# Kernel optimization log

Hardware: AMD Instinct MI355X
Metric: run time of the kernel (lower is better)

The kernel has to match this reference:

```python
import jax, jax.numpy as jnp
import numpy as np

NC = 80
REG = 16          # DFL bins per coordinate
CONF_THRES = 0.25
IOU_THRES = 0.45
MAX_DET = 300
TOPK = 1000       # fixed-size pre-NMS candidate pool (stand-in for max_nms=30000 with A=8400)
MAX_WH = 7680.0   # class offset for class-aware NMS
LEVELS = [(80, 80, 8.0), (40, 40, 16.0), (20, 20, 32.0)]  # (h, w, stride) for imgsz=640


def _make_anchors():
    """make_anchors: grid-cell centers (+0.5 offset) and per-anchor strides."""
    pts, strs = [], []
    for h, w, s in LEVELS:
        sx = jnp.arange(w, dtype=jnp.float32) + 0.5
        sy = jnp.arange(h, dtype=jnp.float32) + 0.5
        gy, gx = jnp.meshgrid(sy, sx, indexing='ij')
        pts.append(jnp.stack([gx, gy], -1).reshape(-1, 2))
        strs.append(jnp.full((h * w,), s, dtype=jnp.float32))
    return jnp.concatenate(pts).T, jnp.concatenate(strs)  # [2, A], [A]


def _box_iou(b):  # b: [K, 4] xyxy -> [K, K] pairwise IoU
    area = (b[:, 2] - b[:, 0]) * (b[:, 3] - b[:, 1])
    lt = jnp.maximum(b[:, None, :2], b[None, :, :2])
    rb = jnp.minimum(b[:, None, 2:], b[None, :, 2:])
    wh = jnp.clip(rb - lt, 0.0)
    inter = wh[..., 0] * wh[..., 1]
    return inter / (area[:, None] + area[None, :] - inter + 1e-7)


def _nms_keep(iou, valid):
    """Greedy NMS over score-sorted candidates: keep[i] iff valid and no earlier kept box overlaps > thr."""
    K = iou.shape[0]
    idx = jnp.arange(K)
    def body(keep, i):
        sup = jnp.any((iou[i] > IOU_THRES) & keep & (idx < i))
        return keep.at[i].set(valid[i] & jnp.logical_not(sup)), None
    keep, _ = jax.lax.scan(body, jnp.zeros(K, dtype=bool), idx)
    return keep


def _forward(preds, dfl_w):
    B, C, A = preds.shape
    # DFL decode: softmax over 16 bins, expectation with arange(16) weights (the 1x1 conv)
    box_logits = preds[:, :4 * REG].reshape(B, 4, REG, A)
    dist = jnp.einsum('bqra,r->bqa', jax.nn.softmax(box_logits, axis=2), dfl_w)  # [B,4,A] ltrb
    anc, strd = _make_anchors()
    lt, rb = dist[:, :2], dist[:, 2:]
    x1y1 = anc[None] - lt
    x2y2 = anc[None] + rb
    c_xy = (x1y1 + x2y2) / 2
    wh = x2y2 - x1y1
    dbox = jnp.concatenate([c_xy, wh], axis=1) * strd  # dist2bbox(xywh) * stride, [B,4,A]
    cls = jax.nn.sigmoid(preds[:, 4 * REG:])           # [B,NC,A]
    # xywh2xyxy
    cx, cy, w, h = dbox[:, 0], dbox[:, 1], dbox[:, 2], dbox[:, 3]
    boxes = jnp.stack([cx - w / 2, cy - h / 2, cx + w / 2, cy + h / 2], axis=-1)  # [B,A,4]
    conf = jnp.max(cls, axis=1)      # [B,A]
    j = jnp.argmax(cls, axis=1)      # [B,A]
    score = jnp.where(conf > CONF_THRES, conf, -1.0)
    top_s, top_i = jax.lax.top_k(score, TOPK)                               # [B,K]
    tb = jnp.take_along_axis(boxes, top_i[..., None], axis=1)               # [B,K,4]
    tj = jnp.take_along_axis(j, top_i, axis=1)                              # [B,K]
    valid = top_s > CONF_THRES
    ob = tb + (tj.astype(preds.dtype) * MAX_WH)[..., None]                  # class-offset boxes
    iou = jax.vmap(_box_iou)(ob)                                            # [B,K,K]
    keep = jax.vmap(_nms_keep)(iou, valid)                                  # [B,K]
    sel = jnp.where(keep, top_s, -1e9)
    order = jnp.argsort(-sel, axis=1)[:, :MAX_DET]                          # kept, score-sorted
    fb = jnp.take_along_axis(tb, order[..., None], axis=1)
    fs = jnp.take_along_axis(top_s, order, axis=1)
    fj = jnp.take_along_axis(tj, order, axis=1).astype(preds.dtype)
    fv = jnp.take_along_axis(keep, order, axis=1)
    out = jnp.concatenate([fb, fs[..., None], fj[..., None]], axis=-1)
    return out * fv[..., None].astype(preds.dtype)                          # [B,300,6]


def setup_inputs() -> dict:
    key = jax.random.key(0)
    k1, _ = jax.random.split(key)
    preds = jax.random.normal(k1, (32, 4 * REG + NC, 8400), dtype=jnp.float32)
    dfl_w = jnp.arange(REG, dtype=jnp.float32)
    return {"preds": preds, "dfl_w": dfl_w}


def reference(preds, dfl_w):
    return _forward(preds, dfl_w)
```

## Files before the change

### kernel.cpp

```cpp
#include <hip/hip_runtime.h>
#include <cstdint>
#include <cstddef>

typedef unsigned long long u64;
typedef unsigned int u32;

#define A_TOT   8400
#define NCLS    80
#define KSLOT   1024
#define NCHUNK  9
#define TOPK_N  1000
#define MAXDET  300
#define OUT_STRIDE (MAXDET * 6)

#define GLOBAL_AS const __attribute__((address_space(1))) void*
#define LDS_AS __attribute__((address_space(3))) void*


__device__ __forceinline__ float sig32(float x) {
#pragma clang fp contract(off)
    float e = (float)exp(-(double)x);
    float t = 1.0f + e;
    return 1.0f / t;
}

__device__ __forceinline__ u32 key_hi_from_score(float s) {
    u32 u = __float_as_uint(s);
    return (u & 0x80000000u) ? ~u : (u | 0x80000000u);
}
__device__ __forceinline__ float score_from_key_hi(u32 t) {
    u32 u = (t & 0x80000000u) ? (t ^ 0x80000000u) : ~t;
    return __uint_as_float(u);
}

__device__ __forceinline__ u64 mp_rank(const u64* A, const u64* B, int t) {
    int lo = 0, hi = t;
    while (lo < hi) {
        int mid = (lo + hi + 1) >> 1;
        if (A[mid - 1] > B[t - mid]) lo = mid; else hi = mid - 1;
    }
    int i = lo, j = t - lo;
    u64 av = A[i], bv = B[j];
    return av > bv ? av : bv;
}

__global__ __launch_bounds__(256) void k_decode(const float* __restrict__ preds,
                                                u64* __restrict__ key_raw,
                                                float4* __restrict__ dbox) {
#pragma clang fp contract(off)
    __shared__ float tile[2][16][256];
    int b = blockIdx.y;
    int a0 = blockIdx.x * 256;
    int t = threadIdx.x;
    int a = a0 + t;
    int nA = A_TOT - a0; if (nA > 256) nA = 256;
    int p4max = nA >> 2;
    const float* pb = preds + (size_t)b * 144 * A_TOT;

    int l  = t & 63;
    int wv = t >> 6;
    int lc = (l < p4max) ? l : (p4max - 1);

    auto stage = [&](int ch0, int buf) {
#pragma unroll
        for (int k = 0; k < 4; ++k) {
            int r = 4 * k + wv;
            const float* gsrc = pb + (size_t)(ch0 + r) * A_TOT + a0 + 4 * lc;
            __builtin_amdgcn_global_load_lds((GLOBAL_AS)gsrc,
                                             (LDS_AS)&tile[buf][r][0],
                                             16, 0, 0);
        }
    };

    float d[4] = {0.f, 0.f, 0.f, 0.f};
    float m = -3.0e38f, m2 = -3.0e38f;
    int jm = 0;

    stage(0, 0);
    __syncthreads();

    for (int cb = 0; cb < 9; ++cb) {
        int buf = cb & 1;
        if (cb + 1 < 9) stage((cb + 1) * 16, (cb + 1) & 1);
        if (t < nA) {
            float x[16];
#pragma unroll
            for (int r = 0; r < 16; ++r) x[r] = tile[buf][r][t];
            if (cb < 4) {
                float mx = x[0];
#pragma unroll
                for (int r = 1; r < 16; ++r) mx = fmaxf(mx, x[r]);
                float e[16], s = 0.f;
#pragma unroll
                for (int r = 0; r < 16; ++r) { e[r] = expf(x[r] - mx); s = s + e[r]; }
                float dd = 0.f;
#pragma unroll
                for (int r = 0; r < 16; ++r) { float pr = e[r] / s; dd = dd + pr * (float)r; }
                d[cb] = dd;
            } else {
                int cbase = (cb - 4) * 16;
#pragma unroll
                for (int r = 0; r < 16; ++r) {
                    int c = cbase + r;
                    float v = x[r];
                    if (v > m) { m2 = m; m = v; jm = c; }
                    else if (v > m2) { m2 = v; }
                }
            }
        }
        if (cb < 8) __syncthreads();
    }

    if (t >= nA) return;

    const float* pc = pb + (size_t)64 * A_TOT + a;
    float conf; int cls = jm;
    if ((m - m2) < 1e-4f || m > 7.0f) {
        float sb = -1.0f; int jb = 0;
        for (int c = 0; c < NCLS; ++c) {
            float s = sig32(pc[(size_t)c * A_TOT]);
            if (s > sb) { sb = s; jb = c; }
        }
        conf = sb; cls = jb;
    } else {
        conf = sig32(m);
    }
    float score = (conf > 0.25f) ? conf : -1.0f;
    u32 hi = key_hi_from_score(score);
    u32 lo = ((0x3FFFu - (u32)a) << 7) | (u32)cls;
    key_raw[(size_t)b * A_TOT + a] = ((u64)hi << 32) | lo;

    int row, col; float stride;
    if (a < 6400)      { row = a / 80;          col = a % 80;          stride = 8.0f; }
    else if (a < 8000) { int aa = a - 6400; row = aa / 40; col = aa % 40; stride = 16.0f; }
    else               { int aa = a - 8000; row = aa / 20; col = aa % 20; stride = 32.0f; }
    float ax = (float)col + 0.5f;
    float ay = (float)row + 0.5f;
    float x1 = ax - d[0], y1 = ay - d[1];
    float x2 = ax + d[2], y2 = ay + d[3];
    float cx = (x1 + x2) / 2.0f, cy = (y1 + y2) / 2.0f;
    float w  = x2 - x1,          h  = y2 - y1;
    float4 db;
    db.x = cx * stride; db.y = cy * stride; db.z = w * stride; db.w = h * stride;
    dbox[(size_t)b * A_TOT + a] = db;
}

__global__ __launch_bounds__(1024) void k_chunksort(const u64* __restrict__ key_raw,
                                                    u64* __restrict__ key_sorted) {
    __shared__ u64 s[KSLOT];
    int b = blockIdx.y, ch = blockIdx.x, t = threadIdx.x;
    int a = ch * KSLOT + t;
    s[t] = (a < A_TOT) ? key_raw[(size_t)b * A_TOT + a] : 0ull;
    __syncthreads();
    for (int k = 2; k <= KSLOT; k <<= 1) {
        for (int j = k >> 1; j > 0; j >>= 1) {
            int ixj = t ^ j;
            if (ixj > t) {
                u64 x = s[t], y = s[ixj];
                bool descBlock = ((t & k) == 0);
                bool sw = descBlock ? (x < y) : (x > y);
                if (sw) { s[t] = y; s[ixj] = x; }
            }
            __syncthreads();
        }
    }
    key_sorted[((size_t)b * NCHUNK + ch) * KSLOT + t] = s[t];
}

__global__ __launch_bounds__(1024) void k_select(const u64* __restrict__ key_sorted,
                                                 u64* __restrict__ topk,
                                                 const float4* __restrict__ dbox,
                                                 float* __restrict__ tb,
                                                 float* __restrict__ ob,
                                                 float* __restrict__ area,
                                                 u32* __restrict__ validf) {
#pragma clang fp contract(off)
    __shared__ u64 L[5 * KSLOT];
    int b = blockIdx.x, t = threadIdx.x;
    const u64* KS = key_sorted + (size_t)b * NCHUNK * KSLOT;

    u64 r0 = mp_rank(KS + 0 * KSLOT, KS + 1 * KSLOT, t);
    u64 r1 = mp_rank(KS + 2 * KSLOT, KS + 3 * KSLOT, t);
    u64 r2 = mp_rank(KS + 4 * KSLOT, KS + 5 * KSLOT, t);
    u64 r3 = mp_rank(KS + 6 * KSLOT, KS + 7 * KSLOT, t);
    u64 r4 = KS[8 * KSLOT + t];
    L[0 * KSLOT + t] = r0; L[1 * KSLOT + t] = r1;
    L[2 * KSLOT + t] = r2; L[3 * KSLOT + t] = r3;
    L[4 * KSLOT + t] = r4;
    __syncthreads();

    u64 m0 = mp_rank(L + 0 * KSLOT, L + 1 * KSLOT, t);
    u64 m1 = mp_rank(L + 2 * KSLOT, L + 3 * KSLOT, t);
    __syncthreads();
    L[0 * KSLOT + t] = m0; L[1 * KSLOT + t] = m1;
    __syncthreads();

    u64 s0 = mp_rank(L + 0 * KSLOT, L + 1 * KSLOT, t);
    __syncthreads();
    L[0 * KSLOT + t] = s0;
    __syncthreads();

    u64 key = mp_rank(L + 0 * KSLOT, L + 4 * KSLOT, t);
    size_t si = (size_t)b * KSLOT + t;
    topk[si] = key;

    u32 hi = (u32)(key >> 32);
    u32 lo = (u32)key;
    bool valid = (t < TOPK_N) && (hi & 0x80000000u);
    if (!valid) {
        tb[si*4+0]=0.f; tb[si*4+1]=0.f; tb[si*4+2]=0.f; tb[si*4+3]=0.f;
        ob[si*4+0]=0.f; ob[si*4+1]=0.f; ob[si*4+2]=0.f; ob[si*4+3]=0.f;
        area[si] = 0.f; validf[si] = 0u;
        return;
    }
    int a   = 0x3FFF - (int)((lo >> 7) & 0x3FFFu);
    int cls = (int)(lo & 0x7Fu);

    float4 db = dbox[(size_t)b * A_TOT + a];
    float bx1 = db.x - db.z / 2.0f, by1 = db.y - db.w / 2.0f;
    float bx2 = db.x + db.z / 2.0f, by2 = db.y + db.w / 2.0f;
    tb[si*4+0] = bx1; tb[si*4+1] = by1; tb[si*4+2] = bx2; tb[si*4+3] = by2;

    float off = (float)cls * 7680.0f;
    float o0 = bx1 + off, o1 = by1 + off, o2 = bx2 + off, o3 = by2 + off;
    ob[si*4+0] = o0; ob[si*4+1] = o1; ob[si*4+2] = o2; ob[si*4+3] = o3;
    area[si] = (o2 - o0) * (o3 - o1);
    validf[si] = 1u;
}

__global__ __launch_bounds__(256) void k_matrix(const float* __restrict__ ob,
                                                const float* __restrict__ area,
                                                u64* __restrict__ masks) {
#pragma clang fp contract(off)
    __shared__ float4 sob[KSLOT];
    __shared__ float  sar[KSLOT];
    int b = blockIdx.y, rblk = blockIdx.x, tid = threadIdx.x;
    const float4* gob = (const float4*)(ob + (size_t)b * KSLOT * 4);
    const float*  gar = area + (size_t)b * KSLOT;
    for (int i = tid; i < KSLOT; i += blockDim.x) { sob[i] = gob[i]; sar[i] = gar[i]; }
    __syncthreads();

    int lane = tid & 63;
    int wave = tid >> 6;
    int i = rblk * 64 + lane;
    float4 bi = sob[i];
    float Ai = sar[i];

#pragma unroll
    for (int wl = 0; wl < 4; ++wl) {
        int w = wave * 4 + wl;
        u64 mword = 0ull;
        if (w >= rblk) {
            for (int bit = 0; bit < 64; ++bit) {
                int j = (w << 6) + bit;
                float4 bj = sob[j];
                float Aj = sar[j];
                float lt0 = fmaxf(bi.x, bj.x);
                float lt1 = fmaxf(bi.y, bj.y);
                float rb0 = fminf(bi.z, bj.z);
                float rb1 = fminf(bi.w, bj.w);
                float ww = fmaxf(rb0 - lt0, 0.0f);
                float hh = fmaxf(rb1 - lt1, 0.0f);
                float inter = ww * hh;
                float den = ((Ai + Aj) - inter) + 1e-7f;
                float iou = inter / den;
                if ((j > i) && (iou > 0.45f)) mword |= (1ull << bit);
            }
        }
        masks[((size_t)b * KSLOT + i) * 16 + w] = mword;
    }
}

__global__ __launch_bounds__(64) void k_scan(const u64* __restrict__ masks,
                                             const u32* __restrict__ validf,
                                             const u64* __restrict__ topk,
                                             const float* __restrict__ tb,
                                             float* __restrict__ out) {
    __shared__ u64 rows[KSLOT];
    __shared__ u64 kw16[16];
    __shared__ int pref[16];
    int b = blockIdx.x, lane = threadIdx.x;
    const char* base = (const char*)(masks + (size_t)b * KSLOT * 16);

    float4 r0, r1, r2, r3, r4, r5, r6, r7;
    {
        const float4* src = (const float4*)base;
        r0 = src[0*64 + lane]; r1 = src[1*64 + lane];
        r2 = src[2*64 + lane]; r3 = src[3*64 + lane];
        r4 = src[4*64 + lane]; r5 = src[5*64 + lane];
        r6 = src[6*64 + lane]; r7 = src[7*64 + lane];
    }

    u64 kw = 0ull;
    u64 rem = 0ull;
    int kept = 0;

    for (int w = 0; w < 16; ++w) {
        {
            float4* dst = (float4*)rows;
            dst[0*64 + lane] = r0; dst[1*64 + lane] = r1;
            dst[2*64 + lane] = r2; dst[3*64 + lane] = r3;
            dst[4*64 + lane] = r4; dst[5*64 + lane] = r5;
            dst[6*64 + lane] = r6; dst[7*64 + lane] = r7;
        }
        u32 vf = validf[(size_t)b * KSLOT + w * 64 + lane];
        u64 valid_w = __ballot(vf != 0u);
        __syncthreads();
        if (w < 15) {
            const float4* src = (const float4*)(base + (size_t)(w + 1) * 8192);
            r0 = src[0*64 + lane]; r1 = src[1*64 + lane];
            r2 = src[2*64 + lane]; r3 = src[3*64 + lane];
            r4 = src[4*64 + lane]; r5 = src[5*64 + lane];
            r6 = src[6*64 + lane]; r7 = src[7*64 + lane];
        }

        u64 live = valid_w & ~__shfl(rem, w);
        while (live) {
            int i = __ffsll(live) - 1;
            if (lane == w) kw |= (1ull << i);
            u64 m = (lane < 16) ? rows[i * 16 + lane] : 0ull;
            rem |= m;
            ++kept;
            if (kept >= MAXDET) break;
            live &= ~(__shfl(m, w) | (1ull << i));
        }
        if (kept >= MAXDET) break;
        __syncthreads();
    }

    if (lane < 16) kw16[lane] = 0ull;
    __syncthreads();
    if (lane < 16) kw16[lane] = kw;
    __syncthreads();
    if (lane == 0) {
        int s = 0;
        for (int w = 0; w < 16; ++w) { pref[w] = s; s += __popcll(kw16[w]); }
    }
    float* outb = out + (size_t)b * OUT_STRIDE;
    for (int z = lane; z < OUT_STRIDE; z += 64) outb[z] = 0.0f;
    __syncthreads();
    for (int w2 = 0; w2 < 16; ++w2) {
        u64 kwv = kw16[w2];
        if ((kwv >> lane) & 1ull) {
            u64 below = (lane == 0) ? 0ull : (kwv & ((1ull << lane) - 1ull));
            int rank = pref[w2] + __popcll(below);
            if (rank < MAXDET) {
                size_t si = (size_t)b * KSLOT + w2 * 64 + lane;
                u64 key = topk[si];
                u32 hi = (u32)(key >> 32);
                u32 lo = (u32)key;
                float score = score_from_key_hi(hi);
                float clsf = (float)(lo & 0x7Fu);
                float* o = outb + rank * 6;
                o[0] = tb[si*4+0]; o[1] = tb[si*4+1];
                o[2] = tb[si*4+2]; o[3] = tb[si*4+3];
                o[4] = score; o[5] = clsf;
            }
        }
    }
}

extern "C" void kernel_launch(void* const* d_in, const int* in_sizes, int n_in,
                              void* d_out, int out_size, void* d_ws, size_t ws_size,
                              hipStream_t stream) {
    const float* preds = (const float*)d_in[0];
    float* out = (float*)d_out;
    int B = in_sizes[0] / (144 * A_TOT);

    char* ws = (char*)d_ws;
    size_t off = 0;
    u64* key_raw    = (u64*)(ws + off); off += (size_t)B * A_TOT * 8;
    u64* key_sorted = (u64*)(ws + off); off += (size_t)B * NCHUNK * KSLOT * 8;
    u64* topk       = (u64*)(ws + off); off += (size_t)B * KSLOT * 8;
    float4* dbox    = (float4*)(ws + off); off += (size_t)B * A_TOT * 16;
    float* tb       = (float*)(ws + off); off += (size_t)B * KSLOT * 4 * 4;
    float* obuf     = (float*)(ws + off); off += (size_t)B * KSLOT * 4 * 4;
    float* area     = (float*)(ws + off); off += (size_t)B * KSLOT * 4;
    u32* validf     = (u32*)(ws + off); off += (size_t)B * KSLOT * 4;
    u64* masks      = (u64*)(ws + off); off += (size_t)B * KSLOT * 16 * 8;

    k_decode<<<dim3((A_TOT + 255) / 256, B), 256, 0, stream>>>(preds, key_raw, dbox);
    k_chunksort<<<dim3(NCHUNK, B), KSLOT, 0, stream>>>(key_raw, key_sorted);
    k_select<<<B, KSLOT, 0, stream>>>(key_sorted, topk, dbox, tb, obuf, area, validf);
    k_matrix<<<dim3(16, B), 256, 0, stream>>>(obuf, area, masks);
    k_scan<<<B, 64, 0, stream>>>(masks, validf, topk, tb, out);
}
```

Baseline: 167.2 us.

## Restructure NMS scan to shuffle intra-word suppression and batch mask ORs

The serial greedy NMS loop in k_scan now keeps each lane's diagonal suppression word in a register and resolves intra-word suppression with a lane shuffle, instead of reading a shared-memory row per kept box. The OR of kept rows into the running removal mask is deferred to after each 64-box word and processed eight rows at a time across lane groups, finished with xor-shuffle reductions. Validity flags are preloaded into shared memory once. The aim is to shorten the latency-bound dependency chain of the serial scan, at the cost of more register pressure and redundant ffs work.

```diff
diff --git a/kernel.cpp b/kernel.cpp
--- a/kernel.cpp
+++ b/kernel.cpp
@@ -277,10 +277,15 @@
                                              const float* __restrict__ tb,
                                              float* __restrict__ out) {
     __shared__ u64 rows[KSLOT];
+    __shared__ u32 vfl[KSLOT];
     __shared__ u64 kw16[16];
     __shared__ int pref[16];
     int b = blockIdx.x, lane = threadIdx.x;
     const char* base = (const char*)(masks + (size_t)b * KSLOT * 16);
+
+#pragma unroll
+    for (int q = 0; q < 16; ++q)
+        vfl[q * 64 + lane] = validf[(size_t)b * KSLOT + q * 64 + lane];
 
     float4 r0, r1, r2, r3, r4, r5, r6, r7;
     {
@@ -291,9 +296,10 @@
         r6 = src[6*64 + lane]; r7 = src[7*64 + lane];
     }
 
-    u64 kw = 0ull;
+    u64 my_kw = 0ull;
     u64 rem = 0ull;
     int kept = 0;
+    bool done = false;
 
     for (int w = 0; w < 16; ++w) {
         {
@@ -303,8 +309,6 @@
             dst[4*64 + lane] = r4; dst[5*64 + lane] = r5;
             dst[6*64 + lane] = r6; dst[7*64 + lane] = r7;
         }
-        u32 vf = validf[(size_t)b * KSLOT + w * 64 + lane];
-        u64 valid_w = __ballot(vf != 0u);
         __syncthreads();
         if (w < 15) {
             const float4* src = (const float4*)(base + (size_t)(w + 1) * 8192);
@@ -314,23 +318,49 @@
             r6 = src[6*64 + lane]; r7 = src[7*64 + lane];
         }
 
+        u32 vf = vfl[w * 64 + lane];
+        u64 valid_w = __ballot(vf != 0u);
+        u64 S = rows[lane * 16 + w];
         u64 live = valid_w & ~__shfl(rem, w);
+        u64 keep_w = 0ull;
         while (live) {
             int i = __ffsll(live) - 1;
-            if (lane == w) kw |= (1ull << i);
-            u64 m = (lane < 16) ? rows[i * 16 + lane] : 0ull;
-            rem |= m;
+            keep_w |= (1ull << i);
             ++kept;
-            if (kept >= MAXDET) break;
-            live &= ~(__shfl(m, w) | (1ull << i));
-        }
-        if (kept >= MAXDET) break;
+            if (kept >= MAXDET) { done = true; break; }
+            live &= ~(__shfl(S, i) | (1ull << i));
+        }
+        if (lane == w) my_kw = keep_w;
+        if (done) break;
+        if (w < 15) {
+            u64 kk = keep_w;
+            while (kk) {
+                int i0 = __ffsll(kk) - 1; kk &= kk - 1;
+                int i1 = i0, i2 = i0, i3 = i0, i4 = i0, i5 = i0, i6 = i0, i7 = i0;
+                if (kk) { i1 = __ffsll(kk) - 1; kk &= kk - 1; }
+                if (kk) { i2 = __ffsll(kk) - 1; kk &= kk - 1; }
+                if (kk) { i3 = __ffsll(kk) - 1; kk &= kk - 1; }
+                if (kk) { i4 = __ffsll(kk) - 1; kk &= kk - 1; }
+                if (kk) { i5 = __ffsll(kk) - 1; kk &= kk - 1; }
+                if (kk) { i6 = __ffsll(kk) - 1; kk &= kk - 1; }
+                if (kk) { i7 = __ffsll(kk) - 1; kk &= kk - 1; }
+                int g = lane >> 4;
+                int igA = (g == 0) ? i0 : (g == 1) ? i1 : (g == 2) ? i2 : i3;
+                int igB = (g == 0) ? i4 : (g == 1) ? i5 : (g == 2) ? i6 : i7;
+                u64 xA = rows[igA * 16 + (lane & 15)];
+                u64 xB = rows[igB * 16 + (lane & 15)];
+                u64 y = xA | xB;
+                y |= __shfl_xor(y, 16);
+                y |= __shfl_xor(y, 32);
+                rem |= y;
+            }
+        }
         __syncthreads();
     }
 
     if (lane < 16) kw16[lane] = 0ull;
     __syncthreads();
-    if (lane < 16) kw16[lane] = kw;
+    if (lane < 16) kw16[lane] = my_kw;
     __syncthreads();
     if (lane == 0) {
         int s = 0;
```

New measurement: 180.7 us. +8.0%, slower.
